# Kernel tuning notes

Hardware: AMD Instinct MI355X
Metric: run time of the kernel (lower is better)

Reference implementation:

```python
import jax, jax.numpy as jnp
import numpy as np

DIM = 128
HEADS = 8
HD = DIM // HEADS          # 16
KS = 8                     # neighborhood kernel size
STRIDE = 2                 # GNA query-group stride
DIL = 2                    # dilation


def axis_indices(L, k, s, d):
    """Per-axis neighborhood indices [L, k] for dilated, strided, edge-clamped NA.

    Queries are grouped in blocks of `s`; every query in a block shares the
    window of the block's center query (GNA 'stride'). Dilation partitions the
    axis into `d` sub-grids; the window lives on the center query's sub-grid
    and is clamped so it never leaves the axis (natten-style sliding window).
    """
    idx = np.zeros((L, k), dtype=np.int32)
    for i in range(L):
        ic = min((i // s) * s + (s - 1) // 2, L - 1)   # group-center query
        r = ic % d                                      # sub-grid (residue)
        Lsub = (L - r + d - 1) // d                     # sub-grid length
        ii = ic // d                                    # index within sub-grid
        start = min(max(ii - (k - 1) // 2, 0), max(Lsub - k, 0))
        for j in range(k):
            idx[i, j] = r + d * min(start + j, Lsub - 1)
    return idx


def setup_inputs() -> dict:
    key = jax.random.key(0)
    ks = jax.random.split(key, 5)
    x = jax.random.normal(ks[0], (1, DIM, 96, 96), jnp.float32)
    # depthwise-grouped qkv conv: Conv2d(dim, 3*dim, 3, 1, 1, groups=dim)
    qkv_w = jax.random.normal(ks[1], (3 * DIM, 1, 3, 3), jnp.float32) * 0.1
    qkv_b = jax.random.normal(ks[2], (3 * DIM,), jnp.float32) * 0.02
    # 1x1 projection: Conv2d(dim, dim, 1)
    proj_w = jax.random.normal(ks[3], (DIM, DIM, 1, 1), jnp.float32) * (DIM ** -0.5)
    proj_b = jax.random.normal(ks[4], (DIM,), jnp.float32) * 0.02
    return {"x": x, "qkv_w": qkv_w, "qkv_b": qkv_b, "proj_w": proj_w, "proj_b": proj_b}


def reference(x, qkv_w, qkv_b, proj_w, proj_b):
    B, C, H, W = x.shape
    # grouped (groups=C) 3x3 conv producing q,k,v
    qkv = jax.lax.conv_general_dilated(
        x, qkv_w, window_strides=(1, 1), padding=[(1, 1), (1, 1)],
        dimension_numbers=("NCHW", "OIHW", "NCHW"), feature_group_count=C)
    qkv = qkv + qkv_b[None, :, None, None]
    qkv = qkv.reshape(B, 3, C, H, W)

    def to_heads(t):  # b c h w -> b h w nh hd
        return t.reshape(B, HEADS, HD, H, W).transpose(0, 3, 4, 1, 2)

    q = to_heads(qkv[:, 0])
    k = to_heads(qkv[:, 1])
    v = to_heads(qkv[:, 2])

    scale = HD ** -0.5
    ri = jnp.asarray(axis_indices(H, KS, STRIDE, DIL))  # [H, KS]
    ci = jnp.asarray(axis_indices(W, KS, STRIDE, DIL))  # [W, KS]
    R = ri[:, :, None, None]       # [H, KS, 1, 1]
    Cc = ci[None, None, :, :]      # [1, 1, W, KS]
    k_win = k[:, R, Cc]            # [B, H, KS, W, KS, nh, hd]
    v_win = v[:, R, Cc]

    logits = jnp.einsum("bijnd,bipjqnd->bijnpq", q * scale, k_win)
    attn = jax.nn.softmax(logits.reshape(B, H, W, HEADS, KS * KS), axis=-1)
    attn = attn.reshape(B, H, W, HEADS, KS, KS)
    out = jnp.einsum("bijnpq,bipjqnd->bijnd", attn, v_win)

    out = out.transpose(0, 3, 4, 1, 2).reshape(B, C, H, W)  # b h w nh hd -> b c h w
    out = jnp.einsum("bchw,oc->bohw", out, proj_w[:, :, 0, 0]) + proj_b[None, :, None, None]
    return out
```

## Files before the change

### kernel.cpp

```cpp
#include <hip/hip_runtime.h>
#include <hip/hip_bf16.h>

#define HH   96
#define WW   96
#define NPIX 9216
#define CH   128
#define NH   8
#define HD   16
#define KS   8

#define NEPIX   2304
#define QTPITCH 136
#define KVTPITCH 264
#define XPITCH  97
#define PPITCH  280

typedef __attribute__((ext_vector_type(8))) short bf16x8;
typedef __attribute__((ext_vector_type(4))) float f32x4;

__device__ __forceinline__ unsigned short f2bf(float f) {
    __hip_bfloat16 b = __float2bfloat16(f);
    union { __hip_bfloat16 b; unsigned short u; } cv; cv.b = b; return cv.u;
}
__device__ __forceinline__ bf16x8 u4_as_bf(uint4 u) {
    union { uint4 u; bf16x8 b; } cv; cv.u = u; return cv.b;
}

__global__ __launch_bounds__(256) void conv_kernel(
    const float* __restrict__ x,
    const float* __restrict__ w,
    const float* __restrict__ bias,
    unsigned short* __restrict__ q_pm,
    unsigned short* __restrict__ k_pm,
    unsigned short* __restrict__ vt_pm)
{
    __shared__ float ldsx[128 * XPITCH];
    __shared__ unsigned short qt [24 * QTPITCH];
    __shared__ unsigned short kvt[12 * KVTPITCH];

    const int row = blockIdx.x >> 2;
    const int qtr = blockIdx.x & 3;
    const int j0q = qtr * 24;
    const int tid = threadIdx.x;
    const int g   = tid >> 1;
    const int sh  = tid & 1;
    const bool kvrow = (row & 1) == 0;

    #pragma unroll
    for (int it = 0; it < 12; ++it) {
        const int t  = it * 256 + tid;
        const int r  = t >> 10;
        const int c  = (t >> 3) & 127;
        const int s4 = t & 7;
        const int rg = row + r - 1;
        const int jj = j0q - 4 + s4 * 4;
        float4 v = make_float4(0.f, 0.f, 0.f, 0.f);
        if (rg >= 0 && rg < HH && jj >= 0 && jj < WW)
            v = *(const float4*)(x + (size_t)c * NPIX + rg * WW + jj);
        *(float4*)&ldsx[c * XPITCH + r * 32 + s4 * 4] = v;
    }
    __syncthreads();

    float xr[3][14];
    {
        const float* xg_l = &ldsx[g * XPITCH + 3 + sh * 12];
        #pragma unroll
        for (int dr = 0; dr < 3; ++dr)
            #pragma unroll
            for (int mm = 0; mm < 14; ++mm)
                xr[dr][mm] = xg_l[dr * 32 + mm];
    }

    #pragma unroll
    for (int dt = 0; dt < 3; ++dt) {
        const int o = 3 * g + dt;
        const int t = o >> 7;
        const int c = o & 127;
        float w9[9];
        #pragma unroll
        for (int k = 0; k < 9; ++k) w9[k] = w[o * 9 + k];
        const float b = bias[o];

        if (t == 0) {
            #pragma unroll
            for (int px = 0; px < 12; ++px) {
                float acc = b;
                #pragma unroll
                for (int kh = 0; kh < 3; ++kh)
                    #pragma unroll
                    for (int kw = 0; kw < 3; ++kw)
                        acc += xr[kh][px + kw] * w9[kh * 3 + kw];
                qt[(sh * 12 + px) * QTPITCH + c] = f2bf(acc);
            }
        } else if (kvrow) {
            #pragma unroll
            for (int pe = 0; pe < 6; ++pe) {
                const int px = pe * 2;
                float acc = b;
                #pragma unroll
                for (int kh = 0; kh < 3; ++kh)
                    #pragma unroll
                    for (int kw = 0; kw < 3; ++kw)
                        acc += xr[kh][px + kw] * w9[kh * 3 + kw];
                kvt[(sh * 6 + pe) * KVTPITCH + (t - 1) * CH + c] = f2bf(acc);
            }
        }
    }

    __syncthreads();

    const int ntask = kvrow ? 1088 : 384;
    #pragma unroll
    for (int it = 0; it < 5; ++it) {
        const int idx = it * 256 + tid;
        if (idx < 384) {
            const int px  = idx >> 4;
            const int c8  = (idx & 15) * 8;
            const uint4 v = *(const uint4*)&qt[px * QTPITCH + c8];
            *(uint4*)(q_pm + ((size_t)(row * WW) + j0q + px) * CH + c8) = v;
        } else if (idx < 576 && kvrow) {
            const int k2  = idx - 384;
            const int epx = k2 >> 4;
            const int c8  = (k2 & 15) * 8;
            const uint4 v = *(const uint4*)&kvt[epx * KVTPITCH + c8];
            *(uint4*)(k_pm + ((size_t)(row >> 1) * 48 + (j0q >> 1) + epx) * CH + c8) = v;
        } else if (idx < ntask) {
            const int v2   = idx - 576;
            const int c    = v2 >> 2;
            const int quad = v2 & 3;
            if (quad < 3) {
                const int e0 = quad * 4;
                const unsigned short* src = &kvt[CH + c];
                const unsigned int a0 =
                    (unsigned int)src[(e0 + 0) * KVTPITCH]
                    | ((unsigned int)src[(e0 + 1) * KVTPITCH] << 16);
                const unsigned int a1 =
                    (unsigned int)src[(e0 + 2) * KVTPITCH]
                    | ((unsigned int)src[(e0 + 3) * KVTPITCH] << 16);
                *(uint2*)(vt_pm + (size_t)c * NEPIX + (row >> 1) * 48
                          + (j0q >> 1) + e0) = make_uint2(a0, a1);
            }
        }
    }
}

__global__ __launch_bounds__(512, 4) void attn_kernel(
    const unsigned short* __restrict__ q_pm,
    const unsigned short* __restrict__ k_pm,
    const unsigned short* __restrict__ vt_pm,
    float* __restrict__ a_t)
{
    __shared__ unsigned short plds[NH][16 * PPITCH];

    const int seg = blockIdx.x;
    const int i   = seg / 6;
    const int j0  = (seg - i * 6) * 16;
    const int er0 = min(max(i / 2 - 3, 0), 40);
    const int ec0 = min(max(j0 / 2 - 3, 0), 40);

    const int tid  = threadIdx.x;
    const int h    = tid >> 6;
    const int lane = tid & 63;
    const int nn   = lane & 15;
    const int g    = lane >> 4;

    const int j   = j0 + nn;
    const int ci0 = min(max(j / 2 - 3, 0), 40) - ec0;

    bf16x8 qf = (bf16x8)(short)0;
    if (g < 2)
        qf = u4_as_bf(*(const uint4*)(q_pm + (size_t)(seg * 16 + nn) * CH
                                      + h * HD + g * 8));
    const f32x4 zacc = {0.f, 0.f, 0.f, 0.f};
    f32x4 st[8];
    #pragma unroll
    for (int t = 0; t < 8; ++t) {
        bf16x8 kf = (bf16x8)(short)0;
        if (g < 2) {
            const int ep = (er0 + t) * 48 + min(ec0 + nn, 47);
            kf = u4_as_bf(*(const uint4*)(k_pm + (size_t)ep * CH
                                          + h * HD + g * 8));
        }
        st[t] = __builtin_amdgcn_mfma_f32_16x16x32_bf16(kf, qf, zacc, 0, 0, 0);
    }

    float m = -1e30f;
    #pragma unroll
    for (int t = 0; t < 8; ++t)
        #pragma unroll
        for (int r = 0; r < 4; ++r) {
            const int cc = g * 4 + r;
            float T = st[t][r] * 0.25f;
            T = ((unsigned)(cc - ci0) < 8u) ? T : -1e30f;
            st[t][r] = T;
            m = fmaxf(m, T);
        }
    m = fmaxf(m, __shfl_xor(m, 16));
    m = fmaxf(m, __shfl_xor(m, 32));

    float s = 0.f;
    #pragma unroll
    for (int t = 0; t < 8; ++t)
        #pragma unroll
        for (int r = 0; r < 4; ++r) {
            const float p = __expf(st[t][r] - m);
            st[t][r] = p;
            s += p;
        }
    s += __shfl_xor(s, 16);
    s += __shfl_xor(s, 32);

    unsigned short* pl = &plds[h][nn * PPITCH];
    const int g4 = g * 4;
    #pragma unroll
    for (int t = 0; t < 8; ++t) {
        const float p0 = st[t][0], p1 = st[t][1], p2 = st[t][2], p3 = st[t][3];
        const unsigned short h0 = f2bf(p0), h1 = f2bf(p1),
                             h2 = f2bf(p2), h3 = f2bf(p3);
        const float r0 = p0 - __uint_as_float((unsigned)h0 << 16);
        const float r1 = p1 - __uint_as_float((unsigned)h1 << 16);
        const float r2 = p2 - __uint_as_float((unsigned)h2 << 16);
        const float r3 = p3 - __uint_as_float((unsigned)h3 << 16);
        const unsigned short l0 = f2bf(r0), l1 = f2bf(r1),
                             l2 = f2bf(r2), l3 = f2bf(r3);
        *(uint2*)&pl[t * 16 + g4] =
            make_uint2((unsigned)h0 | ((unsigned)h1 << 16),
                       (unsigned)h2 | ((unsigned)h3 << 16));
        *(uint2*)&pl[136 + t * 16 + g4] =
            make_uint2((unsigned)l0 | ((unsigned)l1 << 16),
                       (unsigned)l2 | ((unsigned)l3 << 16));
    }

    const unsigned short* vbase = vt_pm + (size_t)(h * HD + nn) * NEPIX;
    const int ecs = ec0 & ~7;
    const int shft = ec0 & 7;
    f32x4 acc = {0.f, 0.f, 0.f, 0.f};
    #pragma unroll
    for (int kt = 0; kt < 4; ++kt) {
        const int vrow = er0 + kt * 2 + (g >> 1);
        const int coff = vrow * 48 + ecs + (g & 1) * 8;
        const uint4 u0 = *(const uint4*)(vbase + coff);
        bf16x8 vf;
        if (shft == 0) {
            vf = u4_as_bf(u0);
        } else {
            const uint4 u1 = *(const uint4*)(vbase + coff + 8);
            const unsigned int s2 = u0.z, s3 = u0.w,
                               s4 = u1.x, s5 = u1.y, s6 = u1.z;
            uint4 o;
            o.x = (s2 >> 16) | (s3 << 16);
            o.y = (s3 >> 16) | (s4 << 16);
            o.z = (s4 >> 16) | (s5 << 16);
            o.w = (s5 >> 16) | (s6 << 16);
            vf = u4_as_bf(o);
        }
        const bf16x8 ph = u4_as_bf(*(const uint4*)&pl[kt * 32 + g * 8]);
        const bf16x8 po = u4_as_bf(*(const uint4*)&pl[136 + kt * 32 + g * 8]);
        acc = __builtin_amdgcn_mfma_f32_16x16x32_bf16(vf, ph, acc, 0, 0, 0);
        acc = __builtin_amdgcn_mfma_f32_16x16x32_bf16(vf, po, acc, 0, 0, 0);
    }

    const float inv = 1.f / s;
    const int pix = seg * 16 + nn;
    #pragma unroll
    for (int r = 0; r < 4; ++r)
        a_t[(size_t)(h * HD + g4 + r) * NPIX + pix] = acc[r] * inv;
}

__global__ __launch_bounds__(256) void proj_kernel(
    const float* __restrict__ a_t,
    const float* __restrict__ pw,
    const float* __restrict__ pb,
    float* __restrict__ out)
{
    __shared__ float at[CH][36];

    const int tid = threadIdx.x;
    const int px0 = blockIdx.x * 32;

    #pragma unroll
    for (int it = 0; it < 4; ++it) {
        const int idx = it * 256 + tid;
        const int c   = idx >> 3;
        const int p4  = (idx & 7) * 4;
        *(float4*)&at[c][p4] =
            *(const float4*)(a_t + (size_t)c * NPIX + px0 + p4);
    }
    __syncthreads();

    const int og = tid >> 3;
    const int o0 = og * 4;
    const int p0 = (tid & 7) * 4;

    float acc[4][4];
    #pragma unroll
    for (int i = 0; i < 4; ++i) {
        const float b = pb[o0 + i];
        #pragma unroll
        for (int jj = 0; jj < 4; ++jj) acc[i][jj] = b;
    }

    #pragma unroll 2
    for (int c0 = 0; c0 < CH; c0 += 4) {
        float4 wv[4];
        #pragma unroll
        for (int i = 0; i < 4; ++i)
            wv[i] = *(const float4*)(pw + (size_t)(o0 + i) * CH + c0);
        float4 av[4];
        #pragma unroll
        for (int k = 0; k < 4; ++k)
            av[k] = *(const float4*)&at[c0 + k][p0];
        #pragma unroll
        for (int i = 0; i < 4; ++i) {
            acc[i][0] += wv[i].x * av[0].x; acc[i][1] += wv[i].x * av[0].y;
            acc[i][2] += wv[i].x * av[0].z; acc[i][3] += wv[i].x * av[0].w;
            acc[i][0] += wv[i].y * av[1].x; acc[i][1] += wv[i].y * av[1].y;
            acc[i][2] += wv[i].y * av[1].z; acc[i][3] += wv[i].y * av[1].w;
            acc[i][0] += wv[i].z * av[2].x; acc[i][1] += wv[i].z * av[2].y;
            acc[i][2] += wv[i].z * av[2].z; acc[i][3] += wv[i].z * av[2].w;
            acc[i][0] += wv[i].w * av[3].x; acc[i][1] += wv[i].w * av[3].y;
            acc[i][2] += wv[i].w * av[3].z; acc[i][3] += wv[i].w * av[3].w;
        }
    }

    #pragma unroll
    for (int i = 0; i < 4; ++i)
        *(float4*)(out + (size_t)(o0 + i) * NPIX + px0 + p0)
            = make_float4(acc[i][0], acc[i][1], acc[i][2], acc[i][3]);
}

extern "C" void kernel_launch(void* const* d_in, const int* in_sizes, int n_in,
                              void* d_out, int out_size, void* d_ws, size_t ws_size,
                              hipStream_t stream)
{
    const float* x      = (const float*)d_in[0];
    const float* qkv_w  = (const float*)d_in[1];
    const float* qkv_b  = (const float*)d_in[2];
    const float* proj_w = (const float*)d_in[3];
    const float* proj_b = (const float*)d_in[4];
    float* out = (float*)d_out;

    unsigned short* vt_pm = (unsigned short*)d_ws;
    unsigned short* q_pm  = vt_pm + (size_t)CH * NEPIX;
    unsigned short* k_pm  = q_pm + (size_t)NPIX * CH;
    float*          a_t   = (float*)(k_pm + (size_t)NEPIX * CH);

    conv_kernel<<<384, 256, 0, stream>>>(x, qkv_w, qkv_b, q_pm, k_pm, vt_pm);
    attn_kernel<<<576, 512, 0, stream>>>(q_pm, k_pm, vt_pm, a_t);
    proj_kernel<<<288, 256, 0, stream>>>(a_t, proj_w, proj_b, out);
}
```

Measured before the change: 95.92 us.

## Retile V into per-head chunked layout, halve conv tiles, reuse P LDS buffer

```diff
diff --git a/kernel.cpp b/kernel.cpp
--- a/kernel.cpp
+++ b/kernel.cpp
@@ -10,10 +10,10 @@
 #define KS   8
 
 #define NEPIX   2304
-#define QTPITCH 136
-#define KVTPITCH 264
-#define XPITCH  97
-#define PPITCH  280
+#define QTP  136
+#define KVTP 264
+#define XP2  61
+#define PP2  72
 
 typedef __attribute__((ext_vector_type(8))) short bf16x8;
 typedef __attribute__((ext_vector_type(4))) float f32x4;
@@ -32,43 +32,46 @@
     const float* __restrict__ bias,
     unsigned short* __restrict__ q_pm,
     unsigned short* __restrict__ k_pm,
-    unsigned short* __restrict__ vt_pm)
+    unsigned short* __restrict__ vt_f)
 {
-    __shared__ float ldsx[128 * XPITCH];
-    __shared__ unsigned short qt [24 * QTPITCH];
-    __shared__ unsigned short kvt[12 * KVTPITCH];
-
-    const int row = blockIdx.x >> 2;
-    const int qtr = blockIdx.x & 3;
-    const int j0q = qtr * 24;
+    __shared__ float ldsx[128 * XP2];
+    __shared__ unsigned short qt [12 * QTP];
+    __shared__ unsigned short kvt[ 6 * KVTP];
+
+    const int row = blockIdx.x >> 3;
+    const int q8  = blockIdx.x & 7;
+    const int j0q = q8 * 12;
     const int tid = threadIdx.x;
     const int g   = tid >> 1;
     const int sh  = tid & 1;
     const bool kvrow = (row & 1) == 0;
 
     #pragma unroll
-    for (int it = 0; it < 12; ++it) {
-        const int t  = it * 256 + tid;
-        const int r  = t >> 10;
-        const int c  = (t >> 3) & 127;
-        const int s4 = t & 7;
-        const int rg = row + r - 1;
-        const int jj = j0q - 4 + s4 * 4;
-        float4 v = make_float4(0.f, 0.f, 0.f, 0.f);
-        if (rg >= 0 && rg < HH && jj >= 0 && jj < WW)
-            v = *(const float4*)(x + (size_t)c * NPIX + rg * WW + jj);
-        *(float4*)&ldsx[c * XPITCH + r * 32 + s4 * 4] = v;
+    for (int it = 0; it < 8; ++it) {
+        const int t = it * 256 + tid;
+        if (t < 1920) {
+            const int r   = t / 640;
+            const int rem = t - r * 640;
+            const int c   = rem / 5;
+            const int s4  = rem - c * 5;
+            const int rg  = row + r - 1;
+            const int jj  = j0q - 4 + s4 * 4;
+            float4 v = make_float4(0.f, 0.f, 0.f, 0.f);
+            if (rg >= 0 && rg < HH && jj >= 0 && jj < WW)
+                v = *(const float4*)(x + (size_t)c * NPIX + rg * WW + jj);
+            *(float4*)&ldsx[c * XP2 + r * 20 + s4 * 4] = v;
+        }
     }
     __syncthreads();
 
-    float xr[3][14];
+    float xr[3][8];
     {
-        const float* xg_l = &ldsx[g * XPITCH + 3 + sh * 12];
+        const float* xg_l = &ldsx[g * XP2 + 3 + sh * 6];
         #pragma unroll
         for (int dr = 0; dr < 3; ++dr)
             #pragma unroll
-            for (int mm = 0; mm < 14; ++mm)
-                xr[dr][mm] = xg_l[dr * 32 + mm];
+            for (int m = 0; m < 8; ++m)
+                xr[dr][m] = xg_l[dr * 20 + m];
     }
 
     #pragma unroll
@@ -83,18 +86,18 @@
 
         if (t == 0) {
             #pragma unroll
-            for (int px = 0; px < 12; ++px) {
+            for (int px = 0; px < 6; ++px) {
                 float acc = b;
                 #pragma unroll
                 for (int kh = 0; kh < 3; ++kh)
                     #pragma unroll
                     for (int kw = 0; kw < 3; ++kw)
                         acc += xr[kh][px + kw] * w9[kh * 3 + kw];
-                qt[(sh * 12 + px) * QTPITCH + c] = f2bf(acc);
+                qt[(sh * 6 + px) * QTP + c] = f2bf(acc);
             }
         } else if (kvrow) {
             #pragma unroll
-            for (int pe = 0; pe < 6; ++pe) {
+            for (int pe = 0; pe < 3; ++pe) {
                 const int px = pe * 2;
                 float acc = b;
                 #pragma unroll
@@ -102,44 +105,49 @@
                     #pragma unroll
                     for (int kw = 0; kw < 3; ++kw)
                         acc += xr[kh][px + kw] * w9[kh * 3 + kw];
-                kvt[(sh * 6 + pe) * KVTPITCH + (t - 1) * CH + c] = f2bf(acc);
+                kvt[(sh * 3 + pe) * KVTP + (t - 1) * CH + c] = f2bf(acc);
             }
         }
     }
 
     __syncthreads();
 
-    const int ntask = kvrow ? 1088 : 384;
-    #pragma unroll
-    for (int it = 0; it < 5; ++it) {
+    const int er = row >> 1;
+    const int b6 = j0q >> 1;
+    const int ntask = kvrow ? ((q8 == 0) ? 800 : 672) : 192;
+    #pragma unroll
+    for (int it = 0; it < 4; ++it) {
         const int idx = it * 256 + tid;
-        if (idx < 384) {
-            const int px  = idx >> 4;
-            const int c8  = (idx & 15) * 8;
-            const uint4 v = *(const uint4*)&qt[px * QTPITCH + c8];
+        if (idx < 192) {
+            const int px = idx >> 4;
+            const int c8 = (idx & 15) * 8;
+            const uint4 v = *(const uint4*)&qt[px * QTP + c8];
             *(uint4*)(q_pm + ((size_t)(row * WW) + j0q + px) * CH + c8) = v;
-        } else if (idx < 576 && kvrow) {
-            const int k2  = idx - 384;
+        } else if (idx < 288 && kvrow) {
+            const int k2  = idx - 192;
             const int epx = k2 >> 4;
             const int c8  = (k2 & 15) * 8;
-            const uint4 v = *(const uint4*)&kvt[epx * KVTPITCH + c8];
-            *(uint4*)(k_pm + ((size_t)(row >> 1) * 48 + (j0q >> 1) + epx) * CH + c8) = v;
+            const uint4 v = *(const uint4*)&kvt[epx * KVTP + c8];
+            *(uint4*)(k_pm + ((size_t)er * 48 + b6 + epx) * CH + c8) = v;
+        } else if (idx < 672 && kvrow) {
+            const int v2 = idx - 288;
+            const int pr = v2 >> 7;
+            const int c  = v2 & 127;
+            const int colA  = b6 + pr * 2;
+            const int chunk = colA >> 3;
+            const int off   = colA & 7;
+            const unsigned int a0 =
+                (unsigned int)kvt[(pr * 2)     * KVTP + CH + c]
+                | ((unsigned int)kvt[(pr * 2 + 1) * KVTP + CH + c] << 16);
+            *(unsigned int*)(vt_f
+                + (((size_t)(c >> 4) * 48 + er) * 7 + chunk) * 128
+                + (c & 15) * 8 + off) = a0;
         } else if (idx < ntask) {
-            const int v2   = idx - 576;
-            const int c    = v2 >> 2;
-            const int quad = v2 & 3;
-            if (quad < 3) {
-                const int e0 = quad * 4;
-                const unsigned short* src = &kvt[CH + c];
-                const unsigned int a0 =
-                    (unsigned int)src[(e0 + 0) * KVTPITCH]
-                    | ((unsigned int)src[(e0 + 1) * KVTPITCH] << 16);
-                const unsigned int a1 =
-                    (unsigned int)src[(e0 + 2) * KVTPITCH]
-                    | ((unsigned int)src[(e0 + 3) * KVTPITCH] << 16);
-                *(uint2*)(vt_pm + (size_t)c * NEPIX + (row >> 1) * 48
-                          + (j0q >> 1) + e0) = make_uint2(a0, a1);
-            }
+            const int zf = idx - 672;
+            const int hh = zf >> 4;
+            const int d  = zf & 15;
+            *(uint4*)(vt_f + (((size_t)hh * 48 + er) * 7 + 6) * 128 + d * 8)
+                = make_uint4(0u, 0u, 0u, 0u);
         }
     }
 }
@@ -147,22 +155,25 @@
 __global__ __launch_bounds__(512, 4) void attn_kernel(
     const unsigned short* __restrict__ q_pm,
     const unsigned short* __restrict__ k_pm,
-    const unsigned short* __restrict__ vt_pm,
+    const unsigned short* __restrict__ vt_f,
     float* __restrict__ a_t)
 {
-    __shared__ unsigned short plds[NH][16 * PPITCH];
+    __shared__ unsigned short plds[NH][16 * PP2];
 
     const int seg = blockIdx.x;
     const int i   = seg / 6;
     const int j0  = (seg - i * 6) * 16;
     const int er0 = min(max(i / 2 - 3, 0), 40);
     const int ec0 = min(max(j0 / 2 - 3, 0), 40);
+    const int ecs = ec0 >> 3;
+    const int sh5 = ec0 & 7;
 
     const int tid  = threadIdx.x;
     const int h    = tid >> 6;
     const int lane = tid & 63;
     const int nn   = lane & 15;
     const int g    = lane >> 4;
+    const int g4   = g * 4;
 
     const int j   = j0 + nn;
     const int ci0 = min(max(j / 2 - 3, 0), 40) - ec0;
@@ -189,7 +200,7 @@
     for (int t = 0; t < 8; ++t)
         #pragma unroll
         for (int r = 0; r < 4; ++r) {
-            const int cc = g * 4 + r;
+            const int cc = g4 + r;
             float T = st[t][r] * 0.25f;
             T = ((unsigned)(cc - ci0) < 8u) ? T : -1e30f;
             st[t][r] = T;
@@ -210,54 +221,69 @@
     s += __shfl_xor(s, 16);
     s += __shfl_xor(s, 32);
 
-    unsigned short* pl = &plds[h][nn * PPITCH];
-    const int g4 = g * 4;
-    #pragma unroll
-    for (int t = 0; t < 8; ++t) {
-        const float p0 = st[t][0], p1 = st[t][1], p2 = st[t][2], p3 = st[t][3];
-        const unsigned short h0 = f2bf(p0), h1 = f2bf(p1),
-                             h2 = f2bf(p2), h3 = f2bf(p3);
-        const float r0 = p0 - __uint_as_float((unsigned)h0 << 16);
-        const float r1 = p1 - __uint_as_float((unsigned)h1 << 16);
-        const float r2 = p2 - __uint_as_float((unsigned)h2 << 16);
-        const float r3 = p3 - __uint_as_float((unsigned)h3 << 16);
-        const unsigned short l0 = f2bf(r0), l1 = f2bf(r1),
-                             l2 = f2bf(r2), l3 = f2bf(r3);
-        *(uint2*)&pl[t * 16 + g4] =
-            make_uint2((unsigned)h0 | ((unsigned)h1 << 16),
-                       (unsigned)h2 | ((unsigned)h3 << 16));
-        *(uint2*)&pl[136 + t * 16 + g4] =
-            make_uint2((unsigned)l0 | ((unsigned)l1 << 16),
-                       (unsigned)l2 | ((unsigned)l3 << 16));
-    }
-
-    const unsigned short* vbase = vt_pm + (size_t)(h * HD + nn) * NEPIX;
-    const int ecs = ec0 & ~7;
-    const int shft = ec0 & 7;
+    unsigned short* pr = &plds[h][nn * PP2];
     f32x4 acc = {0.f, 0.f, 0.f, 0.f};
-    #pragma unroll
-    for (int kt = 0; kt < 4; ++kt) {
-        const int vrow = er0 + kt * 2 + (g >> 1);
-        const int coff = vrow * 48 + ecs + (g & 1) * 8;
-        const uint4 u0 = *(const uint4*)(vbase + coff);
-        bf16x8 vf;
-        if (shft == 0) {
-            vf = u4_as_bf(u0);
-        } else {
-            const uint4 u1 = *(const uint4*)(vbase + coff + 8);
-            const unsigned int s2 = u0.z, s3 = u0.w,
-                               s4 = u1.x, s5 = u1.y, s6 = u1.z;
-            uint4 o;
-            o.x = (s2 >> 16) | (s3 << 16);
-            o.y = (s3 >> 16) | (s4 << 16);
-            o.z = (s4 >> 16) | (s5 << 16);
-            o.w = (s5 >> 16) | (s6 << 16);
-            vf = u4_as_bf(o);
-        }
-        const bf16x8 ph = u4_as_bf(*(const uint4*)&pl[kt * 32 + g * 8]);
-        const bf16x8 po = u4_as_bf(*(const uint4*)&pl[136 + kt * 32 + g * 8]);
-        acc = __builtin_amdgcn_mfma_f32_16x16x32_bf16(vf, ph, acc, 0, 0, 0);
-        acc = __builtin_amdgcn_mfma_f32_16x16x32_bf16(vf, po, acc, 0, 0, 0);
+
+    #pragma unroll
+    for (int hf = 0; hf < 2; ++hf) {
+        #pragma unroll
+        for (int tl = 0; tl < 4; ++tl) {
+            const f32x4 P = st[hf * 4 + tl];
+            const unsigned short a0 = f2bf(P[0]), a1 = f2bf(P[1]),
+                                 a2 = f2bf(P[2]), a3 = f2bf(P[3]);
+            *(uint2*)&pr[tl * 16 + g4] =
+                make_uint2((unsigned)a0 | ((unsigned)a1 << 16),
+                           (unsigned)a2 | ((unsigned)a3 << 16));
+        }
+        bf16x8 vfr[2];
+        #pragma unroll
+        for (int ks = 0; ks < 2; ++ks) {
+            const int tl = ks * 2 + (g >> 1);
+            const int er = er0 + hf * 4 + tl;
+            const int ch = ecs + (g & 1);
+            const unsigned short* vb = vt_f
+                + ((size_t)(h * 48 + er) * 7 + ch) * 128 + nn * 8;
+            const uint4 u0 = *(const uint4*)vb;
+            if (sh5 == 0) {
+                vfr[ks] = u4_as_bf(u0);
+            } else {
+                const uint4 u1 = *(const uint4*)(vb + 128);
+                uint4 o;
+                o.x = (u0.z >> 16) | (u0.w << 16);
+                o.y = (u0.w >> 16) | (u1.x << 16);
+                o.z = (u1.x >> 16) | (u1.y << 16);
+                o.w = (u1.y >> 16) | (u1.z << 16);
+                vfr[ks] = u4_as_bf(o);
+            }
+            const bf16x8 pb =
+                u4_as_bf(*(const uint4*)&pr[tl * 16 + (g & 1) * 8]);
+            acc = __builtin_amdgcn_mfma_f32_16x16x32_bf16(vfr[ks], pb, acc,
+                                                          0, 0, 0);
+        }
+        __builtin_amdgcn_sched_barrier(0);
+        #pragma unroll
+        for (int tl = 0; tl < 4; ++tl) {
+            const f32x4 P = st[hf * 4 + tl];
+            unsigned short lo[4];
+            #pragma unroll
+            for (int r = 0; r < 4; ++r) {
+                const unsigned short hi = f2bf(P[r]);
+                lo[r] = f2bf(P[r] - __uint_as_float((unsigned)hi << 16));
+            }
+            *(uint2*)&pr[tl * 16 + g4] =
+                make_uint2((unsigned)lo[0] | ((unsigned)lo[1] << 16),
+                           (unsigned)lo[2] | ((unsigned)lo[3] << 16));
+        }
+        __builtin_amdgcn_sched_barrier(0);
+        #pragma unroll
+        for (int ks = 0; ks < 2; ++ks) {
+            const int tl = ks * 2 + (g >> 1);
+            const bf16x8 pb =
+                u4_as_bf(*(const uint4*)&pr[tl * 16 + (g & 1) * 8]);
+            acc = __builtin_amdgcn_mfma_f32_16x16x32_bf16(vfr[ks], pb, acc,
+                                                          0, 0, 0);
+        }
+        __builtin_amdgcn_sched_barrier(0);
     }
 
     const float inv = 1.f / s;
@@ -340,12 +366,12 @@
     const float* proj_b = (const float*)d_in[4];
     float* out = (float*)d_out;
 
-    unsigned short* vt_pm = (unsigned short*)d_ws;
-    unsigned short* q_pm  = vt_pm + (size_t)CH * NEPIX;
-    unsigned short* k_pm  = q_pm + (size_t)NPIX * CH;
-    float*          a_t   = (float*)(k_pm + (size_t)NEPIX * CH);
-
-    conv_kernel<<<384, 256, 0, stream>>>(x, qkv_w, qkv_b, q_pm, k_pm, vt_pm);
-    attn_kernel<<<576, 512, 0, stream>>>(q_pm, k_pm, vt_pm, a_t);
+    unsigned short* q_pm = (unsigned short*)d_ws;
+    unsigned short* k_pm = q_pm + (size_t)NPIX * CH;
+    unsigned short* vt_f = k_pm + (size_t)NEPIX * CH;
+    float*          a_t  = (float*)(vt_f + (size_t)8 * 48 * 7 * 128);
+
+    conv_kernel<<<768, 256, 0, stream>>>(x, qkv_w, qkv_b, q_pm, k_pm, vt_f);
+    attn_kernel<<<576, 512, 0, stream>>>(q_pm, k_pm, vt_f, a_t);
     proj_kernel<<<288, 256, 0, stream>>>(a_t, proj_w, proj_b, out);
 }
```

Result: faster. 92.88 us (-3.2%).
